# Performance work log

Measured on AMD Instinct MI355X. Metric: run time of the kernel, lower is better.

The kernel has to match this reference:

```python
import jax, jax.numpy as jnp
import numpy as np

N_EMBD = 1024
HEAD_SIZE = 128
BLOCK_SIZE = 2048
B, T = 8, 2048

def setup_inputs() -> dict:
    key = jax.random.key(0)
    kx, kq, kk, kv = jax.random.split(key, 4)
    x = jax.random.normal(kx, (B, T, N_EMBD), dtype=jnp.float32)
    # nn.Linear(n_embd, head_size, bias=False) weights: [head_size, n_embd]
    s = 1.0 / np.sqrt(N_EMBD)
    Wq = jax.random.uniform(kq, (HEAD_SIZE, N_EMBD), jnp.float32, -s, s)
    Wk = jax.random.uniform(kk, (HEAD_SIZE, N_EMBD), jnp.float32, -s, s)
    Wv = jax.random.uniform(kv, (HEAD_SIZE, N_EMBD), jnp.float32, -s, s)
    return {"x": x, "Wq": Wq, "Wk": Wk, "Wv": Wv}

def reference(x, Wq, Wk, Wv):
    # q,k,v: [B,T,H]
    q = jnp.einsum('btc,hc->bth', x, Wq)
    k = jnp.einsum('btc,hc->bth', x, Wk)
    v = jnp.einsum('btc,hc->bth', x, Wv)
    scale = k.shape[-1] ** -0.5
    wei = jnp.einsum('bth,bsh->bts', q, k) * scale  # [B,T,T]
    Tq = q.shape[1]
    causal = jnp.tril(jnp.ones((Tq, Tq), dtype=bool))
    wei = jnp.where(causal[None, :, :], wei, -jnp.inf)
    wei = jax.nn.softmax(wei, axis=-1)
    out = jnp.einsum('bts,bsh->bth', wei, v)  # [B,T,H]
    return out
```

## Files before the change

### kernel.cpp

```cpp
#include <hip/hip_runtime.h>

#define B_ 8
#define T_ 2048
#define C_ 1024
#define H_ 128
#define BT_ (B_ * T_)

typedef __attribute__((ext_vector_type(8))) short short8;
typedef __attribute__((ext_vector_type(4))) float f32x4;
typedef unsigned short u16;

#define SSCALE 0.12753257708482632f

static __device__ __forceinline__ u16 f2bf(float f) {
    union { float f; unsigned u; } x; x.f = f;
    unsigned r = x.u + 0x7fffu + ((x.u >> 16) & 1u);
    return (u16)(r >> 16);
}

static __device__ __forceinline__ unsigned long long pack4bf(float a, float b, float c, float d) {
    return (unsigned long long)f2bf(a) |
           ((unsigned long long)f2bf(b) << 16) |
           ((unsigned long long)f2bf(c) << 32) |
           ((unsigned long long)f2bf(d) << 48);
}

#define GLDS16(g, l)                                                            \
    __builtin_amdgcn_global_load_lds(                                           \
        (const __attribute__((address_space(1))) void*)(g),                     \
        (__attribute__((address_space(3))) void*)(l), 16, 0, 0)

__global__ __launch_bounds__(256) void wconv_kernel(
    const float* __restrict__ Wq, const float* __restrict__ Wk,
    const float* __restrict__ Wv, u16* __restrict__ wb)
{
    int t = blockIdx.x * 256 + threadIdx.x;
    int e = t * 8;
    const float* __restrict__ src = (e < 131072) ? Wq : (e < 262144 ? Wk : Wv);
    int off = e & 131071;
    float4 f0 = *(const float4*)&src[off];
    float4 f1 = *(const float4*)&src[off + 4];
    union { unsigned long long u[2]; uint4 v; } pk;
    pk.u[0] = pack4bf(f0.x, f0.y, f0.z, f0.w);
    pk.u[1] = pack4bf(f1.x, f1.y, f1.z, f1.w);
    *(uint4*)&wb[e] = pk.v;
}

__global__ __launch_bounds__(256) void proj_kernel(
    const float* __restrict__ x, const u16* __restrict__ wb,
    u16* __restrict__ qo, u16* __restrict__ ko, u16* __restrict__ vt)
{
    __shared__ union {
        struct { u16 a[2][128 * 64]; u16 w[2][128 * 64]; } s;
        u16 c[128 * 132];
    } lds;

    const int tid = threadIdx.x;
    const int lane = tid & 63;
    const int wid = tid >> 6;
    const int m0 = blockIdx.x * 128;
    const int widx = blockIdx.y;
    const u16* __restrict__ W = wb + (size_t)widx * (128 * 1024);

    const int wm = (wid >> 1) * 64;
    const int wn = (wid & 1) * 64;
    const int blr = lane >> 3, bc = lane & 7;

    float4 v[8];

    #pragma unroll
    for (int p = 0; p < 8; p++) {
        int idx = p * 256 + tid, r = idx >> 4, cc = (idx & 15) * 4;
        v[p] = *(const float4*)&x[(size_t)(m0 + r) * C_ + cc];
    }
    #pragma unroll
    for (int jj = 0; jj < 4; jj++) {
        int j = wid * 4 + jj;
        int row = j * 8 + blr;
        GLDS16(W + (size_t)row * C_ + ((bc ^ (row & 7)) * 8),
               (char*)lds.s.w[0] + j * 1024);
    }
    #pragma unroll
    for (int p = 0; p < 8; p++) {
        int idx = p * 256 + tid, r = idx >> 4, cc = (idx & 15) * 4;
        int byte = (r * 128 + cc * 2) ^ ((r & 7) << 4);
        *(unsigned long long*)((char*)lds.s.a[0] + byte) = pack4bf(v[p].x, v[p].y, v[p].z, v[p].w);
    }
    asm volatile("s_waitcnt vmcnt(0) lgkmcnt(0)" ::: "memory");
    __builtin_amdgcn_s_barrier();

    f32x4 acc[4][4];
    #pragma unroll
    for (int i = 0; i < 4; i++)
        #pragma unroll
        for (int j = 0; j < 4; j++) acc[i][j] = f32x4{0.f, 0.f, 0.f, 0.f};

    for (int k = 0; k < 16; k++) {
        const int pb = k & 1;
        const bool pre = (k + 1 < 16);
        if (pre) {
            const int k0n = (k + 1) * 64;
            #pragma unroll
            for (int p = 0; p < 8; p++) {
                int idx = p * 256 + tid, r = idx >> 4, cc = (idx & 15) * 4;
                v[p] = *(const float4*)&x[(size_t)(m0 + r) * C_ + k0n + cc];
            }
            #pragma unroll
            for (int jj = 0; jj < 4; jj++) {
                int j = wid * 4 + jj;
                int row = j * 8 + blr;
                GLDS16(W + (size_t)row * C_ + k0n + ((bc ^ (row & 7)) * 8),
                       (char*)lds.s.w[pb ^ 1] + j * 1024);
            }
        }

        #pragma unroll
        for (int ks = 0; ks < 2; ks++) {
            short8 afrag[4], bfrag[4];
            #pragma unroll
            for (int i = 0; i < 4; i++) {
                int row = wm + i * 16 + (lane & 15);
                int byte = (row * 128 + ks * 64 + (lane >> 4) * 16) ^ ((row & 7) << 4);
                afrag[i] = *(const short8*)((const char*)lds.s.a[pb] + byte);
            }
            #pragma unroll
            for (int j = 0; j < 4; j++) {
                int row = wn + j * 16 + (lane & 15);
                int byte = (row * 128 + ks * 64 + (lane >> 4) * 16) ^ ((row & 7) << 4);
                bfrag[j] = *(const short8*)((const char*)lds.s.w[pb] + byte);
            }
            #pragma unroll
            for (int i = 0; i < 4; i++)
                #pragma unroll
                for (int j = 0; j < 4; j++)
                    acc[i][j] = __builtin_amdgcn_mfma_f32_16x16x32_bf16(
                        afrag[i], bfrag[j], acc[i][j], 0, 0, 0);
        }

        if (pre) {
            #pragma unroll
            for (int p = 0; p < 8; p++) {
                int idx = p * 256 + tid, r = idx >> 4, cc = (idx & 15) * 4;
                int byte = (r * 128 + cc * 2) ^ ((r & 7) << 4);
                *(unsigned long long*)((char*)lds.s.a[pb ^ 1] + byte) =
                    pack4bf(v[p].x, v[p].y, v[p].z, v[p].w);
            }
        }
        asm volatile("s_waitcnt vmcnt(0) lgkmcnt(0)" ::: "memory");
        __builtin_amdgcn_s_barrier();
    }

    const int b = m0 / T_;
    const int tloc = m0 % T_;
    if (widx < 2) {
        u16* __restrict__ dst = (widx == 0) ? qo : ko;
        #pragma unroll
        for (int i = 0; i < 4; i++) {
            int row = m0 + wm + i * 16 + (lane >> 4) * 4;
            #pragma unroll
            for (int j = 0; j < 4; j++) {
                int col = wn + j * 16 + (lane & 15);
                #pragma unroll
                for (int r = 0; r < 4; r++)
                    dst[(size_t)(row + r) * H_ + col] = f2bf(acc[i][j][r]);
            }
        }
    } else {
        __syncthreads();
        #pragma unroll
        for (int i = 0; i < 4; i++) {
            #pragma unroll
            for (int j = 0; j < 4; j++) {
                int colb = wn + j * 16 + (lane & 15);
                #pragma unroll
                for (int r = 0; r < 4; r++) {
                    int rowb = wm + i * 16 + (lane >> 4) * 4 + r;
                    lds.c[rowb * 132 + colb] = f2bf(acc[i][j][r]);
                }
            }
        }
        __syncthreads();
        #pragma unroll
        for (int p = 0; p < 8; p++) {
            int idx = p * 256 + tid;
            int h = idx >> 4, tg = idx & 15;
            u16 pk[8];
            #pragma unroll
            for (int jj = 0; jj < 8; jj++) pk[jj] = lds.c[(tg * 8 + jj) * 132 + h];
            *(short8*)&vt[((size_t)b * H_ + h) * T_ + tloc + tg * 8] = *(const short8*)pk;
        }
    }
}

template<int NSPLIT>
__global__ __launch_bounds__(256) void attn_kernel(
    const u16* __restrict__ q, const u16* __restrict__ k, const u16* __restrict__ vt,
    float* __restrict__ out, float* __restrict__ po1, float* __restrict__ ml)
{
    __shared__ u16 kt[2][64 * 128];
    __shared__ u16 vtt[2][128 * 64];
    __shared__ u16 pl[4][16 * 64];

    const int tid = threadIdx.x, lane = tid & 63, wid = tid >> 6;
    int b, qtile, s0, s1, half = 0;
    if (NSPLIT == 1) {
        int pair = blockIdx.x;
        b = pair & 7; qtile = 31 - (pair >> 3); s0 = 0; s1 = qtile + 1;
    } else {
        int pair = blockIdx.x >> 1; half = blockIdx.x & 1;
        b = pair & 7; int qq = pair >> 3;
        if (half == 0) { qtile = 31 - qq; s0 = 0; s1 = (qtile + 2) >> 1; }
        else           { qtile = qq;      s0 = (qtile + 2) >> 1; s1 = qtile + 1; }
    }
    const int qbase = qtile * 64;

    short8 qf[4];
    const int qrow = qbase + wid * 16 + (lane & 15);
    #pragma unroll
    for (int ks = 0; ks < 4; ks++)
        qf[ks] = *(const short8*)&q[((size_t)b * T_ + qrow) * H_ + ks * 32 + (lane >> 4) * 8];

    f32x4 oacc[8];
    #pragma unroll
    for (int i = 0; i < 8; i++) oacc[i] = f32x4{0.f, 0.f, 0.f, 0.f};
    float mrow[4], lrow[4];
    #pragma unroll
    for (int r = 0; r < 4; r++) { mrow[r] = -1e30f; lrow[r] = 0.f; }

    const u16* __restrict__ kb = k + (size_t)b * T_ * H_;
    const u16* __restrict__ vb = vt + (size_t)b * H_ * T_;

    auto stage = [&](int s, int pbuf) {
        const int kvbase = s * 64;
        #pragma unroll
        for (int jj = 0; jj < 4; jj++) {
            int j = wid * 4 + jj;
            int r = j * 4 + (lane >> 4), c = lane & 15;
            GLDS16(kb + (size_t)(kvbase + r) * H_ + ((c ^ (r & 7)) * 8),
                   (char*)kt[pbuf] + j * 1024);
        }
        #pragma unroll
        for (int jj = 0; jj < 4; jj++) {
            int j = wid * 4 + jj;
            int h = j * 8 + (lane >> 3), c = lane & 7;
            GLDS16(vb + (size_t)h * T_ + kvbase + ((c ^ (h & 7)) * 8),
                   (char*)vtt[pbuf] + j * 1024);
        }
    };

    if (s0 < s1) {
        stage(s0, 0);
        asm volatile("s_waitcnt vmcnt(0)" ::: "memory");
        __builtin_amdgcn_s_barrier();
    }

    for (int s = s0; s < s1; s++) {
        const int pb = (s - s0) & 1;
        if (s + 1 < s1) stage(s + 1, pb ^ 1);
        const int kvbase = s * 64;

        f32x4 sacc[4];
        #pragma unroll
        for (int nt = 0; nt < 4; nt++) sacc[nt] = f32x4{0.f, 0.f, 0.f, 0.f};
        #pragma unroll
        for (int ks = 0; ks < 4; ks++) {
            #pragma unroll
            for (int nt = 0; nt < 4; nt++) {
                int row = nt * 16 + (lane & 15);
                int byte = (row * 256 + ks * 64 + (lane >> 4) * 16) ^ ((row & 7) << 4);
                short8 bfr = *(const short8*)((const char*)kt[pb] + byte);
                sacc[nt] = __builtin_amdgcn_mfma_f32_16x16x32_bf16(qf[ks], bfr, sacc[nt], 0, 0, 0);
            }
        }

        if (s == qtile) {
            #pragma unroll
            for (int nt = 0; nt < 4; nt++) {
                int colg = kvbase + nt * 16 + (lane & 15);
                #pragma unroll
                for (int r = 0; r < 4; r++) {
                    int rowg = qbase + wid * 16 + (lane >> 4) * 4 + r;
                    if (colg > rowg) sacc[nt][r] = -1e30f;
                }
            }
        }

        float scalef[4];
        #pragma unroll
        for (int r = 0; r < 4; r++) {
            float mx = fmaxf(fmaxf(sacc[0][r], sacc[1][r]), fmaxf(sacc[2][r], sacc[3][r]));
            #pragma unroll
            for (int off = 1; off < 16; off <<= 1)
                mx = fmaxf(mx, __shfl_xor(mx, off, 16));
            float mnew = fmaxf(mrow[r], mx);
            scalef[r] = exp2f((mrow[r] - mnew) * SSCALE);
            mrow[r] = mnew;
        }
        float psum[4] = {0.f, 0.f, 0.f, 0.f};
        #pragma unroll
        for (int nt = 0; nt < 4; nt++) {
            #pragma unroll
            for (int r = 0; r < 4; r++) {
                float pv = exp2f((sacc[nt][r] - mrow[r]) * SSCALE);
                psum[r] += pv;
                int row = (lane >> 4) * 4 + r;
                int byte = (row * 128 + (nt * 16 + (lane & 15)) * 2) ^ ((row & 7) << 4);
                *(u16*)((char*)pl[wid] + byte) = f2bf(pv);
            }
        }
        #pragma unroll
        for (int r = 0; r < 4; r++) {
            #pragma unroll
            for (int off = 1; off < 16; off <<= 1)
                psum[r] += __shfl_xor(psum[r], off, 16);
            lrow[r] = lrow[r] * scalef[r] + psum[r];
        }
        #pragma unroll
        for (int i = 0; i < 8; i++)
            #pragma unroll
            for (int r = 0; r < 4; r++) oacc[i][r] *= scalef[r];

        #pragma unroll
        for (int ks = 0; ks < 2; ks++) {
            int arow = lane & 15;
            int abyte = (arow * 128 + ks * 64 + (lane >> 4) * 16) ^ ((arow & 7) << 4);
            short8 af = *(const short8*)((const char*)pl[wid] + abyte);
            #pragma unroll
            for (int nt2 = 0; nt2 < 8; nt2++) {
                int vrow = nt2 * 16 + (lane & 15);
                int vbyte = (vrow * 128 + ks * 64 + (lane >> 4) * 16) ^ ((vrow & 7) << 4);
                short8 bfr = *(const short8*)((const char*)vtt[pb] + vbyte);
                oacc[nt2] = __builtin_amdgcn_mfma_f32_16x16x32_bf16(af, bfr, oacc[nt2], 0, 0, 0);
            }
        }

        asm volatile("s_waitcnt vmcnt(0)" ::: "memory");
        __builtin_amdgcn_s_barrier();
    }

    if (NSPLIT == 1) {
        #pragma unroll
        for (int nt2 = 0; nt2 < 8; nt2++)
            #pragma unroll
            for (int r = 0; r < 4; r++) {
                int rowg = qbase + wid * 16 + (lane >> 4) * 4 + r;
                out[((size_t)b * T_ + rowg) * H_ + nt2 * 16 + (lane & 15)] = oacc[nt2][r] / lrow[r];
            }
    } else {
        float* __restrict__ dst = (half == 0) ? out : po1;
        #pragma unroll
        for (int nt2 = 0; nt2 < 8; nt2++)
            #pragma unroll
            for (int r = 0; r < 4; r++) {
                int rowg = qbase + wid * 16 + (lane >> 4) * 4 + r;
                dst[((size_t)b * T_ + rowg) * H_ + nt2 * 16 + (lane & 15)] = oacc[nt2][r];
            }
        if ((lane & 15) == 0) {
            #pragma unroll
            for (int r = 0; r < 4; r++) {
                int rowg = qbase + wid * 16 + (lane >> 4) * 4 + r;
                ml[(half * 2 + 0) * BT_ + b * T_ + rowg] = mrow[r];
                ml[(half * 2 + 1) * BT_ + b * T_ + rowg] = lrow[r];
            }
        }
    }
}

__global__ __launch_bounds__(256) void combine_kernel(
    float* __restrict__ out, const float* __restrict__ po1, const float* __restrict__ ml)
{
    int i = blockIdx.x * 256 + threadIdx.x;
    int row = i >> 5;
    float m0 = ml[row],           l0 = ml[BT_ + row];
    float m1 = ml[2 * BT_ + row], l1 = ml[3 * BT_ + row];
    float mx = fmaxf(m0, m1);
    float w0 = exp2f((m0 - mx) * SSCALE), w1 = exp2f((m1 - mx) * SSCALE);
    float inv = 1.0f / (w0 * l0 + w1 * l1);
    float4 a = ((const float4*)out)[i];
    float4 c = ((const float4*)po1)[i];
    float4 r;
    r.x = (a.x * w0 + c.x * w1) * inv;
    r.y = (a.y * w0 + c.y * w1) * inv;
    r.z = (a.z * w0 + c.z * w1) * inv;
    r.w = (a.w * w0 + c.w * w1) * inv;
    ((float4*)out)[i] = r;
}

extern "C" void kernel_launch(void* const* d_in, const int* in_sizes, int n_in,
                              void* d_out, int out_size, void* d_ws, size_t ws_size,
                              hipStream_t stream) {
    const float* x  = (const float*)d_in[0];
    const float* Wq = (const float*)d_in[1];
    const float* Wk = (const float*)d_in[2];
    const float* Wv = (const float*)d_in[3];

    u16* q  = (u16*)d_ws;
    u16* kk = q + (size_t)BT_ * H_;
    u16* vt = kk + (size_t)BT_ * H_;
    u16* wb = vt + (size_t)BT_ * H_;
    const size_t po1_off = (size_t)3 * BT_ * H_ * 2 + 393216 * 2;
    float* po1 = (float*)((char*)d_ws + po1_off);
    float* ml  = (float*)((char*)d_ws + po1_off + (size_t)BT_ * H_ * 4);
    const size_t need2 = po1_off + (size_t)BT_ * H_ * 4 + (size_t)4 * BT_ * 4;

    wconv_kernel<<<192, 256, 0, stream>>>(Wq, Wk, Wv, wb);
    proj_kernel<<<dim3(128, 3), 256, 0, stream>>>(x, wb, q, kk, vt);
    if (ws_size >= need2) {
        attn_kernel<2><<<512, 256, 0, stream>>>(q, kk, vt, (float*)d_out, po1, ml);
        combine_kernel<<<2048, 256, 0, stream>>>((float*)d_out, po1, ml);
    } else {
        attn_kernel<1><<<256, 256, 0, stream>>>(q, kk, vt, (float*)d_out, nullptr, nullptr);
    }
}
```

Baseline: 188.4 us.

## Fuse QKV projection into one 64x384 tile per block and prioritize attention MFMAs

The projection kernel now computes all three of Q, K and V for a 64-row tile in one 512-thread block, instead of launching a separate 128x128 block per weight matrix. Each x tile is read from global memory and converted to bf16 only once rather than three times. The V transpose goes through LDS as before. The attention kernel also raises wave priority around its MFMA sections via s_setprio. In exchange, LDS use per block grows with the 384-row weight tile, and the grid becomes 256 blocks of 512 threads.

```diff
diff --git a/kernel.cpp b/kernel.cpp
--- a/kernel.cpp
+++ b/kernel.cpp
@@ -46,54 +46,53 @@
     *(uint4*)&wb[e] = pk.v;
 }
 
-__global__ __launch_bounds__(256) void proj_kernel(
+__global__ __launch_bounds__(512) void proj_kernel(
     const float* __restrict__ x, const u16* __restrict__ wb,
     u16* __restrict__ qo, u16* __restrict__ ko, u16* __restrict__ vt)
 {
     __shared__ union {
-        struct { u16 a[2][128 * 64]; u16 w[2][128 * 64]; } s;
-        u16 c[128 * 132];
+        struct { u16 a[2][64 * 64]; u16 w[2][384 * 64]; } s;
+        u16 c[64 * 136];
     } lds;
 
     const int tid = threadIdx.x;
     const int lane = tid & 63;
     const int wid = tid >> 6;
-    const int m0 = blockIdx.x * 128;
-    const int widx = blockIdx.y;
-    const u16* __restrict__ W = wb + (size_t)widx * (128 * 1024);
-
-    const int wm = (wid >> 1) * 64;
-    const int wn = (wid & 1) * 64;
-    const int blr = lane >> 3, bc = lane & 7;
-
-    float4 v[8];
-
-    #pragma unroll
-    for (int p = 0; p < 8; p++) {
-        int idx = p * 256 + tid, r = idx >> 4, cc = (idx & 15) * 4;
-        v[p] = *(const float4*)&x[(size_t)(m0 + r) * C_ + cc];
-    }
-    #pragma unroll
-    for (int jj = 0; jj < 4; jj++) {
-        int j = wid * 4 + jj;
-        int row = j * 8 + blr;
-        GLDS16(W + (size_t)row * C_ + ((bc ^ (row & 7)) * 8),
+    const int wr = wid >> 2;
+    const int wc = wid & 3;
+    const int m0 = blockIdx.x * 64;
+
+    const int gr = lane >> 3, gc = lane & 7;
+
+    float4 va[2];
+
+    f32x4 acc[2][6];
+    #pragma unroll
+    for (int i = 0; i < 2; i++)
+        #pragma unroll
+        for (int j = 0; j < 6; j++) acc[i][j] = f32x4{0.f, 0.f, 0.f, 0.f};
+
+    #pragma unroll
+    for (int p = 0; p < 2; p++) {
+        int idx = p * 512 + tid, r = idx >> 4, cc = (idx & 15) * 4;
+        va[p] = *(const float4*)&x[(size_t)(m0 + r) * C_ + cc];
+    }
+    #pragma unroll
+    for (int jj = 0; jj < 6; jj++) {
+        int j = wid * 6 + jj;
+        int row = j * 8 + gr;
+        GLDS16(wb + (size_t)row * C_ + ((gc ^ gr) * 8),
                (char*)lds.s.w[0] + j * 1024);
     }
     #pragma unroll
-    for (int p = 0; p < 8; p++) {
-        int idx = p * 256 + tid, r = idx >> 4, cc = (idx & 15) * 4;
+    for (int p = 0; p < 2; p++) {
+        int idx = p * 512 + tid, r = idx >> 4, cc = (idx & 15) * 4;
         int byte = (r * 128 + cc * 2) ^ ((r & 7) << 4);
-        *(unsigned long long*)((char*)lds.s.a[0] + byte) = pack4bf(v[p].x, v[p].y, v[p].z, v[p].w);
+        *(unsigned long long*)((char*)lds.s.a[0] + byte) =
+            pack4bf(va[p].x, va[p].y, va[p].z, va[p].w);
     }
     asm volatile("s_waitcnt vmcnt(0) lgkmcnt(0)" ::: "memory");
     __builtin_amdgcn_s_barrier();
-
-    f32x4 acc[4][4];
-    #pragma unroll
-    for (int i = 0; i < 4; i++)
-        #pragma unroll
-        for (int j = 0; j < 4; j++) acc[i][j] = f32x4{0.f, 0.f, 0.f, 0.f};
 
     for (int k = 0; k < 16; k++) {
         const int pb = k & 1;
@@ -101,49 +100,49 @@
         if (pre) {
             const int k0n = (k + 1) * 64;
             #pragma unroll
-            for (int p = 0; p < 8; p++) {
-                int idx = p * 256 + tid, r = idx >> 4, cc = (idx & 15) * 4;
-                v[p] = *(const float4*)&x[(size_t)(m0 + r) * C_ + k0n + cc];
-            }
-            #pragma unroll
-            for (int jj = 0; jj < 4; jj++) {
-                int j = wid * 4 + jj;
-                int row = j * 8 + blr;
-                GLDS16(W + (size_t)row * C_ + k0n + ((bc ^ (row & 7)) * 8),
+            for (int p = 0; p < 2; p++) {
+                int idx = p * 512 + tid, r = idx >> 4, cc = (idx & 15) * 4;
+                va[p] = *(const float4*)&x[(size_t)(m0 + r) * C_ + k0n + cc];
+            }
+            #pragma unroll
+            for (int jj = 0; jj < 6; jj++) {
+                int j = wid * 6 + jj;
+                int row = j * 8 + gr;
+                GLDS16(wb + (size_t)row * C_ + k0n + ((gc ^ gr) * 8),
                        (char*)lds.s.w[pb ^ 1] + j * 1024);
             }
         }
 
         #pragma unroll
         for (int ks = 0; ks < 2; ks++) {
-            short8 afrag[4], bfrag[4];
-            #pragma unroll
-            for (int i = 0; i < 4; i++) {
-                int row = wm + i * 16 + (lane & 15);
+            short8 af[2], bf[6];
+            #pragma unroll
+            for (int i = 0; i < 2; i++) {
+                int row = wr * 32 + i * 16 + (lane & 15);
                 int byte = (row * 128 + ks * 64 + (lane >> 4) * 16) ^ ((row & 7) << 4);
-                afrag[i] = *(const short8*)((const char*)lds.s.a[pb] + byte);
-            }
-            #pragma unroll
-            for (int j = 0; j < 4; j++) {
-                int row = wn + j * 16 + (lane & 15);
-                int byte = (row * 128 + ks * 64 + (lane >> 4) * 16) ^ ((row & 7) << 4);
-                bfrag[j] = *(const short8*)((const char*)lds.s.w[pb] + byte);
-            }
-            #pragma unroll
-            for (int i = 0; i < 4; i++)
+                af[i] = *(const short8*)((const char*)lds.s.a[pb] + byte);
+            }
+            #pragma unroll
+            for (int j = 0; j < 6; j++) {
+                int n = wc * 96 + j * 16 + (lane & 15);
+                int byte = (n * 128 + ks * 64 + (lane >> 4) * 16) ^ ((n & 7) << 4);
+                bf[j] = *(const short8*)((const char*)lds.s.w[pb] + byte);
+            }
+            #pragma unroll
+            for (int i = 0; i < 2; i++)
                 #pragma unroll
-                for (int j = 0; j < 4; j++)
+                for (int j = 0; j < 6; j++)
                     acc[i][j] = __builtin_amdgcn_mfma_f32_16x16x32_bf16(
-                        afrag[i], bfrag[j], acc[i][j], 0, 0, 0);
+                        af[i], bf[j], acc[i][j], 0, 0, 0);
         }
 
         if (pre) {
             #pragma unroll
-            for (int p = 0; p < 8; p++) {
-                int idx = p * 256 + tid, r = idx >> 4, cc = (idx & 15) * 4;
+            for (int p = 0; p < 2; p++) {
+                int idx = p * 512 + tid, r = idx >> 4, cc = (idx & 15) * 4;
                 int byte = (r * 128 + cc * 2) ^ ((r & 7) << 4);
                 *(unsigned long long*)((char*)lds.s.a[pb ^ 1] + byte) =
-                    pack4bf(v[p].x, v[p].y, v[p].z, v[p].w);
+                    pack4bf(va[p].x, va[p].y, va[p].z, va[p].w);
             }
         }
         asm volatile("s_waitcnt vmcnt(0) lgkmcnt(0)" ::: "memory");
@@ -152,43 +151,36 @@
 
     const int b = m0 / T_;
     const int tloc = m0 % T_;
-    if (widx < 2) {
-        u16* __restrict__ dst = (widx == 0) ? qo : ko;
-        #pragma unroll
-        for (int i = 0; i < 4; i++) {
-            int row = m0 + wm + i * 16 + (lane >> 4) * 4;
-            #pragma unroll
-            for (int j = 0; j < 4; j++) {
-                int col = wn + j * 16 + (lane & 15);
+    #pragma unroll
+    for (int i = 0; i < 2; i++) {
+        #pragma unroll
+        for (int j = 0; j < 6; j++) {
+            int n = wc * 96 + j * 16 + (lane & 15);
+            int wdx = n >> 7;
+            int rowb = wr * 32 + i * 16 + (lane >> 4) * 4;
+            if (wdx < 2) {
+                u16* __restrict__ dst = wdx ? ko : qo;
+                int col = n & 127;
                 #pragma unroll
                 for (int r = 0; r < 4; r++)
-                    dst[(size_t)(row + r) * H_ + col] = f2bf(acc[i][j][r]);
-            }
-        }
-    } else {
-        __syncthreads();
-        #pragma unroll
-        for (int i = 0; i < 4; i++) {
-            #pragma unroll
-            for (int j = 0; j < 4; j++) {
-                int colb = wn + j * 16 + (lane & 15);
+                    dst[(size_t)(m0 + rowb + r) * H_ + col] = f2bf(acc[i][j][r]);
+            } else {
+                int h = n - 256;
                 #pragma unroll
-                for (int r = 0; r < 4; r++) {
-                    int rowb = wm + i * 16 + (lane >> 4) * 4 + r;
-                    lds.c[rowb * 132 + colb] = f2bf(acc[i][j][r]);
-                }
-            }
-        }
-        __syncthreads();
-        #pragma unroll
-        for (int p = 0; p < 8; p++) {
-            int idx = p * 256 + tid;
-            int h = idx >> 4, tg = idx & 15;
-            u16 pk[8];
-            #pragma unroll
-            for (int jj = 0; jj < 8; jj++) pk[jj] = lds.c[(tg * 8 + jj) * 132 + h];
-            *(short8*)&vt[((size_t)b * H_ + h) * T_ + tloc + tg * 8] = *(const short8*)pk;
-        }
+                for (int r = 0; r < 4; r++)
+                    lds.c[(rowb + r) * 136 + h] = f2bf(acc[i][j][r]);
+            }
+        }
+    }
+    __syncthreads();
+    #pragma unroll
+    for (int p = 0; p < 2; p++) {
+        int idx = p * 512 + tid;
+        int h = idx >> 3, tg = idx & 7;
+        u16 pk[8];
+        #pragma unroll
+        for (int jj = 0; jj < 8; jj++) pk[jj] = lds.c[(tg * 8 + jj) * 136 + h];
+        *(short8*)&vt[((size_t)b * H_ + h) * T_ + tloc + tg * 8] = *(const short8*)pk;
     }
 }
 
@@ -262,6 +254,7 @@
         f32x4 sacc[4];
         #pragma unroll
         for (int nt = 0; nt < 4; nt++) sacc[nt] = f32x4{0.f, 0.f, 0.f, 0.f};
+        __builtin_amdgcn_s_setprio(1);
         #pragma unroll
         for (int ks = 0; ks < 4; ks++) {
             #pragma unroll
@@ -272,6 +265,7 @@
                 sacc[nt] = __builtin_amdgcn_mfma_f32_16x16x32_bf16(qf[ks], bfr, sacc[nt], 0, 0, 0);
             }
         }
+        __builtin_amdgcn_s_setprio(0);
 
         if (s == qtile) {
             #pragma unroll
@@ -320,6 +314,7 @@
             #pragma unroll
             for (int r = 0; r < 4; r++) oacc[i][r] *= scalef[r];
 
+        __builtin_amdgcn_s_setprio(1);
         #pragma unroll
         for (int ks = 0; ks < 2; ks++) {
             int arow = lane & 15;
@@ -333,6 +328,7 @@
                 oacc[nt2] = __builtin_amdgcn_mfma_f32_16x16x32_bf16(af, bfr, oacc[nt2], 0, 0, 0);
             }
         }
+        __builtin_amdgcn_s_setprio(0);
 
         asm volatile("s_waitcnt vmcnt(0)" ::: "memory");
         __builtin_amdgcn_s_barrier();
@@ -404,7 +400,7 @@
     const size_t need2 = po1_off + (size_t)BT_ * H_ * 4 + (size_t)4 * BT_ * 4;
 
     wconv_kernel<<<192, 256, 0, stream>>>(Wq, Wk, Wv, wb);
-    proj_kernel<<<dim3(128, 3), 256, 0, stream>>>(x, wb, q, kk, vt);
+    proj_kernel<<<256, 512, 0, stream>>>(x, wb, q, kk, vt);
     if (ws_size >= need2) {
         attn_kernel<2><<<512, 256, 0, stream>>>(q, kk, vt, (float*)d_out, po1, ml);
         combine_kernel<<<2048, 256, 0, stream>>>((float*)d_out, po1, ml);
```

New measurement: 168.0 us. 1.12x faster.
